# Kernel optimization log

Measured on AMD Instinct MI355X. Metric: run time of the kernel, lower is better.

The kernel has to match this reference:

```python
import jax, jax.numpy as jnp
import numpy as np

N, E, G = 10000, 80000, 32
Z, C, B, H = 10, 128, 8, 64
R_MAX = 5.0
AVG_NEIGH = 16.0
L_OFF = [0, 1, 4, 9, 16]  # slice offsets for l = 0..3 blocks of the SH vector


def real_sh(u):
    # Real spherical harmonics up to l=3, 'component' normalization (sum_m Y_lm^2 = 2l+1)
    x, y, z = u[:, 0], u[:, 1], u[:, 2]
    s3, s5, s15 = 3.0 ** 0.5, 5.0 ** 0.5, 15.0 ** 0.5
    cols = [
        jnp.ones_like(x),
        s3 * x, s3 * y, s3 * z,
        s15 * x * y, s15 * y * z, (s5 / 2) * (3 * z ** 2 - 1),
        s15 * x * z, (s15 / 2) * (x ** 2 - y ** 2),
        (70.0 ** 0.5 / 4) * (3 * x ** 2 * y - y ** 3),
        105.0 ** 0.5 * x * y * z,
        (42.0 ** 0.5 / 4) * y * (5 * z ** 2 - 1),
        (7.0 ** 0.5 / 2) * (5 * z ** 3 - 3 * z),
        (42.0 ** 0.5 / 4) * x * (5 * z ** 2 - 1),
        (105.0 ** 0.5 / 2) * z * (x ** 2 - y ** 2),
        (70.0 ** 0.5 / 4) * (x ** 3 - 3 * x * y ** 2),
    ]
    return jnp.stack(cols, axis=-1)  # [E, 16]


def poly_cutoff(x, p=5):
    f = (1.0 - (p + 1) * (p + 2) / 2 * x ** p
         + p * (p + 2) * x ** (p + 1)
         - p * (p + 1) / 2 * x ** (p + 2))
    return f * (x < 1.0).astype(f.dtype)


def setup_inputs() -> dict:
    key = jax.random.key(0)
    ks = jax.random.split(key, 20)
    vectors = jax.random.normal(ks[0], (E, 3), dtype=jnp.float32) * 1.5
    elem = jax.random.randint(ks[1], (N,), 0, Z)
    node_attrs = jax.nn.one_hot(elem, Z, dtype=jnp.float32)
    edge_index = jax.random.randint(ks[2], (2, E), 0, N).astype(jnp.int64)
    batch = jnp.sort(jax.random.randint(ks[3], (N,), 0, G)).astype(jnp.int64)

    def init(k, shape, fan_in):
        return jax.random.normal(k, shape, dtype=jnp.float32) / np.sqrt(fan_in)

    return {
        "vectors": vectors,
        "node_attrs": node_attrs,
        "W_embed": init(ks[4], (Z, C), Z),
        "atomic_energies": -jnp.arange(1, Z + 1, dtype=jnp.float32),
        "rw1": init(ks[5], (2, B, H), B),
        "rw2": init(ks[6], (2, H, H), H),
        "rw3": init(ks[7], (2, H, H), H),
        "rw4": init(ks[8], (2, H, 4 * C), H),
        "Wmix": init(ks[9], (2, 4, C, C), C),
        "U": init(ks[10], (2, Z, 4), Z),
        "Wprod": init(ks[11], (2, C, C), C),
        "Wsc": init(ks[12], (2, C, C), C),
        "Wro0": init(ks[13], (C, 1), C),
        "Wro1a": init(ks[14], (C, 16), C),
        "Wro1b": init(ks[15], (16, 1), 16),
        "scale": jnp.array([1.0], dtype=jnp.float32),
        "shift": jnp.array([0.0], dtype=jnp.float32),
        "edge_index": edge_index,
        "batch": batch,
    }


def reference(vectors, node_attrs, W_embed, atomic_energies, rw1, rw2, rw3, rw4,
              Wmix, U, Wprod, Wsc, Wro0, Wro1a, Wro1b, scale, shift,
              edge_index, batch):
    sender, receiver = edge_index[0], edge_index[1]
    r = jnp.linalg.norm(vectors, axis=-1)                     # [E]
    u = vectors / r[:, None]
    Y = real_sh(u)                                            # [E, 16]
    n = jnp.arange(1, B + 1, dtype=vectors.dtype)
    bessel = jnp.sqrt(2.0 / R_MAX) * jnp.sin(n[None] * jnp.pi * r[:, None] / R_MAX) / r[:, None]
    edge_feats = bessel * poly_cutoff(r / R_MAX)[:, None]     # [E, B]

    h = node_attrs @ W_embed                                  # [N, C] node embedding
    node_e0 = node_attrs @ atomic_energies                    # [N] atomic reference energies
    e0 = jax.ops.segment_sum(node_e0, batch, num_segments=G)  # [G]

    node_inter = jnp.zeros((node_attrs.shape[0],), dtype=vectors.dtype)
    for i in range(2):  # interaction layers (fixed small count)
        f = jax.nn.silu(edge_feats @ rw1[i])
        f = jax.nn.silu(f @ rw2[i])
        f = jax.nn.silu(f @ rw3[i])
        R_w = (f @ rw4[i]).reshape(-1, 4, C)                  # [E, 4, C] radial weights per l-path
        hs = h[sender]                                        # [E, C] edge gather
        A_parts = []
        for l in range(4):
            # channelwise tensor product (uvu): scalar node feats x Y_l -> l
            m = (R_w[:, l, :] * hs)[:, :, None] * Y[:, None, L_OFF[l]:L_OFF[l + 1]]  # [E, C, 2l+1]
            agg = jax.ops.segment_sum(m, receiver, num_segments=node_attrs.shape[0]) / AVG_NEIGH
            A_parts.append(jnp.einsum('ncm,cd->ndm', agg, Wmix[i, l]))
        # product basis: rotation-invariant powers per l, element-dependent contraction
        inv = jnp.stack([(p ** 2).sum(-1) for p in A_parts], axis=-1)  # [N, C, 4]
        w = node_attrs @ U[i]                                          # [N, 4]
        h = jnp.einsum('ncl,nl->nc', inv, w) @ Wprod[i] + h @ Wsc[i]   # product + residual sc
        if i == 0:
            node_inter = node_inter + (h @ Wro0)[:, 0]                 # linear readout
        else:
            node_inter = node_inter + (jax.nn.silu(h @ Wro1a) @ Wro1b)[:, 0]  # nonlinear readout
    node_inter = scale[0] * node_inter + shift[0]                       # scale-shift
    total = e0 + jax.ops.segment_sum(node_inter, batch, num_segments=G)
    return total  # [G] per-graph energies
```

## Files before the change

### kernel.cpp

```cpp
#include <hip/hip_runtime.h>

#define NN 10000
#define NE 80000
#define NG 32
#define NZ 10
#define NC 128
#define RMAXF 5.0f

typedef _Float16 f16;
typedef _Float16 half8 __attribute__((ext_vector_type(8)));
typedef float f32x4 __attribute__((ext_vector_type(4)));

__device__ __forceinline__ float silu_f(float x) {
    return x / (1.0f + __expf(-x));
}

__device__ __forceinline__ int clampi(int v, int lo, int hi) {
    return v < lo ? lo : (v > hi ? hi : v);
}

__device__ __forceinline__ uint4 pack8f(float4 a, float4 b) {
    union { f16 h[8]; uint4 u; } P;
    P.h[0] = (f16)a.x; P.h[1] = (f16)a.y; P.h[2] = (f16)a.z; P.h[3] = (f16)a.w;
    P.h[4] = (f16)b.x; P.h[5] = (f16)b.y; P.h[6] = (f16)b.z; P.h[7] = (f16)b.w;
    return P.u;
}

__global__ void zero_stuff(int* counts, int* cursor, float* out) {
    int i = blockIdx.x * blockDim.x + threadIdx.x;
    if (i < NN) { counts[i] = 0; cursor[i] = 0; }
    if (i < NG) out[i] = 0.0f;
}

__global__ void prep_weights(const float* __restrict__ Wmix, const float* __restrict__ Wprod,
                             const float* __restrict__ Wsc,
                             const float* __restrict__ rw2, const float* __restrict__ rw3,
                             const float* __restrict__ rw4,
                             f16* __restrict__ WmixT, f16* __restrict__ WprodT, f16* __restrict__ WscT,
                             f16* __restrict__ w2T, f16* __restrict__ w3T, f16* __restrict__ w4T) {
    int i = blockIdx.x * blockDim.x + threadIdx.x;
    if (i < 2 * 4 * 128 * 128) {
        int cc = i & 127, d = (i >> 7) & 127, g = i >> 14;
        WmixT[i] = (f16)Wmix[((size_t)g * 128 + cc) * 128 + d];
    }
    if (i < 2 * 128 * 128) {
        int cc = i & 127, d = (i >> 7) & 127, g = i >> 14;
        WprodT[i] = (f16)Wprod[((size_t)g * 128 + cc) * 128 + d];
        WscT[i]   = (f16)Wsc[((size_t)g * 128 + cc) * 128 + d];
    }
    if (i < 2 * 512 * 64) {
        int k = i & 63, j = (i >> 6) & 511, ly = i >> 15;
        w4T[i] = (f16)rw4[((size_t)ly * 64 + k) * 512 + j];
    }
    if (i < 2 * 64 * 64) {
        int k = i & 63, j = (i >> 6) & 63, ly = i >> 12;
        w2T[i] = (f16)rw2[((size_t)ly * 64 + k) * 64 + j];
        w3T[i] = (f16)rw3[((size_t)ly * 64 + k) * 64 + j];
    }
}

__global__ void node_init(const float* __restrict__ attrs, const float* __restrict__ W_embed,
                          const float* __restrict__ ae, const float* __restrict__ U,
                          float* __restrict__ h, float* __restrict__ node_e0, float* __restrict__ wU) {
    int gid = blockIdx.x * blockDim.x + threadIdx.x;
    if (gid >= NN * NC) return;
    int n = gid >> 7, c = gid & 127;
    float a[NZ];
#pragma unroll
    for (int z = 0; z < NZ; z++) a[z] = attrs[n * NZ + z];
    float acc = 0.f;
#pragma unroll
    for (int z = 0; z < NZ; z++) acc += a[z] * W_embed[z * NC + c];
    h[(size_t)n * NC + c] = acc;
    if (c == 0) {
        float e = 0.f;
#pragma unroll
        for (int z = 0; z < NZ; z++) e += a[z] * ae[z];
        node_e0[n] = e;
    }
    if (c < 8) {
        int i = c >> 2, l = c & 3;
        float s = 0.f;
#pragma unroll
        for (int z = 0; z < NZ; z++) s += a[z] * U[i * NZ * 4 + z * 4 + l];
        wU[(size_t)i * NN * 4 + n * 4 + l] = s;
    }
}

__global__ void edge_geom(const float* __restrict__ vec, float* __restrict__ Y, float* __restrict__ ef) {
    int e = blockIdx.x * blockDim.x + threadIdx.x;
    if (e >= NE) return;
    float vx = vec[e * 3 + 0], vy = vec[e * 3 + 1], vz = vec[e * 3 + 2];
    float r = sqrtf(vx * vx + vy * vy + vz * vz);
    float inv = 1.0f / r;
    float x = vx * inv, y = vy * inv, z = vz * inv;
    const float s3 = 1.7320508075688772f;
    const float s5 = 2.23606797749979f;
    const float s15 = 3.872983346207417f;
    const float c9 = 2.091650066335189f;
    const float c10 = 10.246950765959598f;
    const float c11 = 1.6201851746019651f;
    const float c12 = 1.3228756555322954f;
    const float c14 = 5.123475382979799f;
    float o[16];
    o[0] = 1.0f;
    o[1] = s3 * x; o[2] = s3 * y; o[3] = s3 * z;
    o[4] = s15 * x * y; o[5] = s15 * y * z; o[6] = 0.5f * s5 * (3.f * z * z - 1.f);
    o[7] = s15 * x * z; o[8] = 0.5f * s15 * (x * x - y * y);
    o[9] = c9 * (3.f * x * x * y - y * y * y);
    o[10] = c10 * x * y * z;
    o[11] = c11 * y * (5.f * z * z - 1.f);
    o[12] = c12 * (5.f * z * z * z - 3.f * z);
    o[13] = c11 * x * (5.f * z * z - 1.f);
    o[14] = c14 * z * (x * x - y * y);
    o[15] = c9 * (x * x * x - 3.f * x * y * y);
#pragma unroll
    for (int m = 0; m < 16; m++) Y[(size_t)e * 16 + m] = o[m];
    float xc = r / RMAXF;
    float cut = 0.0f;
    if (xc < 1.0f) {
        float x5 = xc * xc * xc * xc * xc;
        cut = 1.0f - 21.0f * x5 + 35.0f * x5 * xc - 15.0f * x5 * xc * xc;
    }
    float pref = sqrtf(2.0f / RMAXF) * inv * cut;
#pragma unroll
    for (int b = 0; b < 8; b++) {
        float arg = (float)(b + 1) * 3.14159265358979323846f * r / RMAXF;
        ef[(size_t)e * 8 + b] = pref * sinf(arg);
    }
}

__global__ void hist_recv(const int* __restrict__ recv, int* __restrict__ counts) {
    int e = blockIdx.x * blockDim.x + threadIdx.x;
    if (e < NE) atomicAdd(&counts[clampi(recv[e], 0, NN - 1)], 1);
}

__global__ void scan_counts(const int* __restrict__ counts, int* __restrict__ rowstart) {
    __shared__ int part[1024];
    int t = threadIdx.x;
    const int CH = 10;
    int base = t * CH;
    int loc[CH];
    int s = 0;
#pragma unroll
    for (int j = 0; j < CH; j++) {
        int v = (base + j < NN) ? counts[base + j] : 0;
        loc[j] = s; s += v;
    }
    part[t] = s;
    __syncthreads();
    for (int off = 1; off < 1024; off <<= 1) {
        int v = (t >= off) ? part[t - off] : 0;
        __syncthreads();
        part[t] += v;
        __syncthreads();
    }
    int chunk = (t > 0) ? part[t - 1] : 0;
#pragma unroll
    for (int j = 0; j < CH; j++)
        if (base + j < NN) rowstart[base + j] = chunk + loc[j];
    if (t == 0) rowstart[NN] = part[1023];
}

__global__ void scatter_edges(const int* __restrict__ recv, const int* __restrict__ rowstart,
                              int* __restrict__ cursor, int* __restrict__ elist) {
    int e = blockIdx.x * blockDim.x + threadIdx.x;
    if (e < NE) {
        int r = clampi(recv[e], 0, NN - 1);
        int p = atomicAdd(&cursor[r], 1);
        int slot = clampi(rowstart[r] + p, 0, NE - 1);
        elist[slot] = e;
    }
}

__global__ __launch_bounds__(256) void edge_mlp(const float* __restrict__ ef,
                                                const float* __restrict__ w1,
                                                const f16* __restrict__ w2T, const f16* __restrict__ w3T,
                                                const f16* __restrict__ w4T,
                                                f16* __restrict__ Rw) {
    __shared__ __align__(16) char L[8192 * 2 + 16384];
    char* X1 = L;
    char* X2 = L + 8192;
    char* X4 = L + 16384;

    int tid = threadIdx.x;
    int lane = tid & 63;
    int w = tid >> 6;
    int ln = lane & 15, kq = lane >> 4;
    int eb = blockIdx.x * 64;

    {
        int jb = w * 16;
        const float4* efv = (const float4*)(ef + (size_t)(eb + lane) * 8);
        float4 ea = efv[0], eb4 = efv[1];
        float in8[8] = {ea.x, ea.y, ea.z, ea.w, eb4.x, eb4.y, eb4.z, eb4.w};
        f16 pk[16];
#pragma unroll
        for (int j = 0; j < 16; j++) {
            float a = 0.f;
#pragma unroll
            for (int b = 0; b < 8; b++) a += in8[b] * w1[b * 64 + jb + j];
            pk[j] = (f16)silu_f(a);
        }
        int base = lane * 128 + jb * 2;
#pragma unroll
        for (int t = 0; t < 2; t++) {
            int byte = (base + t * 16) ^ ((lane & 7) << 4);
            *(uint4*)(X1 + byte) = ((uint4*)pk)[t];
        }
    }
    __syncthreads();

    {
        half8 a[2];
#pragma unroll
        for (int kc = 0; kc < 2; kc++) {
            int byte = ((w * 16 + ln) * 128 + kc * 64 + kq * 16) ^ ((ln & 7) << 4);
            a[kc] = *(const half8*)(X1 + byte);
        }
#pragma unroll
        for (int nt = 0; nt < 4; nt++) {
            f32x4 acc = {0.f, 0.f, 0.f, 0.f};
#pragma unroll
            for (int kc = 0; kc < 2; kc++) {
                half8 b = *(const half8*)(w2T + (nt * 16 + ln) * 64 + kc * 32 + kq * 8);
                acc = __builtin_amdgcn_mfma_f32_16x16x32_f16(a[kc], b, acc, 0, 0, 0);
            }
#pragma unroll
            for (int r = 0; r < 4; r++) {
                int row = w * 16 + kq * 4 + r;
                int byte = (row * 128 + (nt * 16 + ln) * 2) ^ ((row & 7) << 4);
                *(f16*)(X2 + byte) = (f16)silu_f(acc[r]);
            }
        }
    }
    __syncthreads();

    {
        half8 a[2];
#pragma unroll
        for (int kc = 0; kc < 2; kc++) {
            int byte = ((w * 16 + ln) * 128 + kc * 64 + kq * 16) ^ ((ln & 7) << 4);
            a[kc] = *(const half8*)(X2 + byte);
        }
#pragma unroll
        for (int nt = 0; nt < 4; nt++) {
            f32x4 acc = {0.f, 0.f, 0.f, 0.f};
#pragma unroll
            for (int kc = 0; kc < 2; kc++) {
                half8 b = *(const half8*)(w3T + (nt * 16 + ln) * 64 + kc * 32 + kq * 8);
                acc = __builtin_amdgcn_mfma_f32_16x16x32_f16(a[kc], b, acc, 0, 0, 0);
            }
#pragma unroll
            for (int r = 0; r < 4; r++) {
                int row = w * 16 + kq * 4 + r;
                int byte = (row * 128 + (nt * 16 + ln) * 2) ^ ((row & 7) << 4);
                *(f16*)(X1 + byte) = (f16)silu_f(acc[r]);
            }
        }
    }
    __syncthreads();

    half8 a3[2];
#pragma unroll
    for (int kc = 0; kc < 2; kc++) {
        int byte = ((w * 16 + ln) * 128 + kc * 64 + kq * 16) ^ ((ln & 7) << 4);
        a3[kc] = *(const half8*)(X1 + byte);
    }
    for (int q = 0; q < 4; q++) {
#pragma unroll
        for (int nt = 0; nt < 8; nt++) {
            f32x4 acc = {0.f, 0.f, 0.f, 0.f};
#pragma unroll
            for (int kc = 0; kc < 2; kc++) {
                half8 b = *(const half8*)(w4T + ((q * 8 + nt) * 16 + ln) * 64 + kc * 32 + kq * 8);
                acc = __builtin_amdgcn_mfma_f32_16x16x32_f16(a3[kc], b, acc, 0, 0, 0);
            }
#pragma unroll
            for (int r = 0; r < 4; r++) {
                int row = w * 16 + kq * 4 + r;
                int byte = (row * 256 + (nt * 16 + ln) * 2) ^ ((row & 15) << 4);
                *(f16*)(X4 + byte) = (f16)acc[r];
            }
        }
#pragma unroll
        for (int it = 0; it < 4; it++) {
            int i = it * 64 + lane;
            int row = w * 16 + (i >> 4);
            int chunk = i & 15;
            int byte = (row * 256 + chunk * 16) ^ ((row & 15) << 4);
            uint4 v = *(const uint4*)(X4 + byte);
            *(uint4*)(Rw + (size_t)(eb + row) * 512 + q * 128 + chunk * 8) = v;
        }
    }
}

__global__ __launch_bounds__(256) void agg_only(const int* __restrict__ rowstart, const int* __restrict__ elist,
                                                const int* __restrict__ send, const float* __restrict__ h_in,
                                                const f16* __restrict__ Rw, const float* __restrict__ Y,
                                                f16* __restrict__ aggH) {
    __shared__ int eL[64], sL[64];
    int n = blockIdx.x, tid = threadIdx.x;
    int c = tid & 127, mh = tid >> 7;
    float acc[8];
#pragma unroll
    for (int q = 0; q < 8; q++) acc[q] = 0.f;
    int beg = rowstart[n], end = rowstart[n + 1];
    for (int base = beg; base < end; base += 64) {
        int cnt = min(64, end - base);
        __syncthreads();
        if (tid < cnt) {
            int e = clampi(elist[base + tid], 0, NE - 1);
            eL[tid] = e;
            sL[tid] = clampi(send[e], 0, NN - 1);
        }
        __syncthreads();
        for (int idx = 0; idx < cnt; idx++) {
            int e = eL[idx];
            int s = sL[idx];
            float hs = h_in[(size_t)s * NC + c];
            const f16* rwp = Rw + (size_t)e * 512;
            float y[8];
#pragma unroll
            for (int q = 0; q < 8; q++) y[q] = Y[(size_t)e * 16 + mh * 8 + q];
            if (mh == 0) {
                float p0 = (float)rwp[c] * hs;
                float p1 = (float)rwp[128 + c] * hs;
                float p2 = (float)rwp[256 + c] * hs;
                acc[0] += p0 * y[0];
                acc[1] += p1 * y[1]; acc[2] += p1 * y[2]; acc[3] += p1 * y[3];
                acc[4] += p2 * y[4]; acc[5] += p2 * y[5]; acc[6] += p2 * y[6]; acc[7] += p2 * y[7];
            } else {
                float p2 = (float)rwp[256 + c] * hs;
                float p3 = (float)rwp[384 + c] * hs;
                acc[0] += p2 * y[0];
#pragma unroll
                for (int q = 1; q < 8; q++) acc[q] += p3 * y[q];
            }
        }
    }
    const float inv16 = 1.0f / 16.0f;
#pragma unroll
    for (int q = 0; q < 8; q++)
        aggH[(size_t)n * 2048 + (size_t)(mh * 8 + q) * NC + c] = (f16)(acc[q] * inv16);
}

__global__ __launch_bounds__(256) void mix_mfma(
    const f16* __restrict__ aggH, const f16* __restrict__ WmixT,
    const float* __restrict__ wU, const float* __restrict__ h_in,
    const f16* __restrict__ WprodT, const f16* __restrict__ WscT,
    const float* __restrict__ Wro0, const float* __restrict__ Wro1a, const float* __restrict__ Wro1b,
    float* __restrict__ h_out, float* __restrict__ ni, int layer)
{
    __shared__ __align__(16) char Lb[65536 + 8192 + 256 + 1024];
    float* invwL = (float*)(Lb + 65536);
    float* wUL   = (float*)(Lb + 65536 + 8192);
    float* p16L  = (float*)(Lb + 65536 + 8192 + 256);
    f16* houtH   = (f16*)(Lb + 65536);

    int tid = threadIdx.x;
    int nb = blockIdx.x * 16;
    int lane = tid & 63;
    int w = tid >> 6;
    int ln = lane & 15, kq = lane >> 4;

    {
        const uint4* src = (const uint4*)(aggH + (size_t)nb * 2048);
        for (int i = tid; i < 4096; i += 256) {
            int byte = i * 16;
            int node = byte >> 12;
            int sw = byte ^ ((node & 7) << 4);
            *(uint4*)(Lb + sw) = src[i];
        }
    }
    if (tid < 64) wUL[tid] = wU[(size_t)nb * 4 + tid];
    for (int i = tid; i < 2048; i += 256) invwL[i] = 0.f;
    __syncthreads();

    float invwacc[32];
#pragma unroll
    for (int i = 0; i < 32; i++) invwacc[i] = 0.f;
#pragma unroll
    for (int i = 0; i < 4; i++) {
        int m = w * 4 + i;
        int l = (m == 0) ? 0 : (m < 4) ? 1 : (m < 9) ? 2 : 3;
        half8 a[4];
#pragma unroll
        for (int k = 0; k < 4; k++) {
            int byte = (ln * 16 + m) * 256 + (k * 32 + kq * 8) * 2;
            byte ^= (ln & 7) << 4;
            a[k] = *(const half8*)(Lb + byte);
        }
        const f16* Bt = WmixT + ((size_t)(layer * 4 + l) << 14);
#pragma unroll
        for (int nt = 0; nt < 8; nt++) {
            f32x4 acc = {0.f, 0.f, 0.f, 0.f};
#pragma unroll
            for (int k = 0; k < 4; k++) {
                half8 b = *(const half8*)(Bt + (nt * 16 + ln) * 128 + k * 32 + kq * 8);
                acc = __builtin_amdgcn_mfma_f32_16x16x32_f16(a[k], b, acc, 0, 0, 0);
            }
#pragma unroll
            for (int r = 0; r < 4; r++) {
                int nd = kq * 4 + r;
                float v = acc[r];
                invwacc[nt * 4 + r] += v * v * wUL[nd * 4 + l];
            }
        }
    }
#pragma unroll
    for (int nt = 0; nt < 8; nt++)
#pragma unroll
        for (int r = 0; r < 4; r++)
            atomicAdd(&invwL[(kq * 4 + r) * 128 + nt * 16 + ln], invwacc[nt * 4 + r]);
    __syncthreads();

    {
        int node = tid >> 4, ch = tid & 15;
        int byte = (node * 256 + ch * 16) ^ ((node & 7) << 4);
        float4 v0 = *(float4*)&invwL[node * 128 + ch * 8];
        float4 v1 = *(float4*)&invwL[node * 128 + ch * 8 + 4];
        *(uint4*)(Lb + byte) = pack8f(v0, v1);
        const float4* hp = (const float4*)(h_in + (size_t)(nb + node) * 128 + ch * 8);
        float4 g0 = hp[0], g1 = hp[1];
        *(uint4*)(Lb + 4096 + byte) = pack8f(g0, g1);
    }
    __syncthreads();

    {
        half8 ai[4], ah[4];
#pragma unroll
        for (int k = 0; k < 4; k++) {
            int byte = (ln * 256 + (k * 32 + kq * 8) * 2) ^ ((ln & 7) << 4);
            ai[k] = *(const half8*)(Lb + byte);
            ah[k] = *(const half8*)(Lb + 4096 + byte);
        }
        const f16* Bp = WprodT + ((size_t)layer << 14);
        const f16* Bs = WscT + ((size_t)layer << 14);
#pragma unroll
        for (int j = 0; j < 2; j++) {
            int nt = w * 2 + j;
            f32x4 acc = {0.f, 0.f, 0.f, 0.f};
#pragma unroll
            for (int k = 0; k < 4; k++) {
                half8 b = *(const half8*)(Bp + (nt * 16 + ln) * 128 + k * 32 + kq * 8);
                acc = __builtin_amdgcn_mfma_f32_16x16x32_f16(ai[k], b, acc, 0, 0, 0);
            }
#pragma unroll
            for (int k = 0; k < 4; k++) {
                half8 b = *(const half8*)(Bs + (nt * 16 + ln) * 128 + k * 32 + kq * 8);
                acc = __builtin_amdgcn_mfma_f32_16x16x32_f16(ah[k], b, acc, 0, 0, 0);
            }
#pragma unroll
            for (int r = 0; r < 4; r++) {
                int node = kq * 4 + r;
                int d = nt * 16 + ln;
                h_out[(size_t)(nb + node) * 128 + d] = acc[r];
                houtH[node * 128 + d] = (f16)acc[r];
            }
        }
    }
    __syncthreads();

    int rn = tid >> 4, rj = tid & 15;
    if (layer == 0) {
        float s = 0.f;
        for (int cc = rj; cc < 128; cc += 16) s += (float)houtH[rn * 128 + cc] * Wro0[cc];
        p16L[tid] = s;
    } else {
        float s = 0.f;
        for (int cc = 0; cc < 128; cc++) s += (float)houtH[rn * 128 + cc] * Wro1a[cc * 16 + rj];
        s = silu_f(s);
        p16L[tid] = s * Wro1b[rj];
    }
    __syncthreads();
    if (tid < 16) {
        float t = 0.f;
#pragma unroll
        for (int j = 0; j < 16; j++) t += p16L[tid * 16 + j];
        ni[nb + tid] = (layer == 0) ? t : (ni[nb + tid] + t);
    }
}

__global__ void finalize(const float* __restrict__ node_e0, const float* __restrict__ ni,
                         const int* __restrict__ batch, const float* __restrict__ scale,
                         const float* __restrict__ shift, float* __restrict__ out) {
    __shared__ float bins[NG];
    int tid = threadIdx.x;
    if (tid < NG) bins[tid] = 0.f;
    __syncthreads();
    int n = blockIdx.x * blockDim.x + tid;
    if (n < NN) {
        float v = node_e0[n] + scale[0] * ni[n] + shift[0];
        atomicAdd(&bins[clampi(batch[n], 0, NG - 1)], v);
    }
    __syncthreads();
    if (tid < NG) atomicAdd(&out[tid], bins[tid]);
}

extern "C" void kernel_launch(void* const* d_in, const int* in_sizes, int n_in,
                              void* d_out, int out_size, void* d_ws, size_t ws_size,
                              hipStream_t stream) {
    (void)in_sizes; (void)n_in; (void)out_size; (void)ws_size;
    const float* vectors = (const float*)d_in[0];
    const float* attrs   = (const float*)d_in[1];
    const float* W_embed = (const float*)d_in[2];
    const float* ae      = (const float*)d_in[3];
    const float* rw1     = (const float*)d_in[4];
    const float* rw2     = (const float*)d_in[5];
    const float* rw3     = (const float*)d_in[6];
    const float* rw4     = (const float*)d_in[7];
    const float* Wmix    = (const float*)d_in[8];
    const float* U       = (const float*)d_in[9];
    const float* Wprod   = (const float*)d_in[10];
    const float* Wsc     = (const float*)d_in[11];
    const float* Wro0    = (const float*)d_in[12];
    const float* Wro1a   = (const float*)d_in[13];
    const float* Wro1b   = (const float*)d_in[14];
    const float* scale   = (const float*)d_in[15];
    const float* shift   = (const float*)d_in[16];
    const int* eidx      = (const int*)d_in[17];
    const int* batch     = (const int*)d_in[18];
    float* out = (float*)d_out;

    char* w = (char*)d_ws;
    size_t off = 0;
    auto alloc = [&](size_t bytes) -> void* {
        void* p = (void*)(w + off);
        off += (bytes + 255) & ~(size_t)255;
        return p;
    };
    float* Y       = (float*)alloc((size_t)NE * 16 * 4);
    float* ef      = (float*)alloc((size_t)NE * 8 * 4);
    f16*   Rw      = (f16*)  alloc((size_t)NE * 512 * 2);
    f16*   aggH    = (f16*)  alloc((size_t)NN * 2048 * 2);
    float* hA      = (float*)alloc((size_t)NN * NC * 4);
    float* hB      = (float*)alloc((size_t)NN * NC * 4);
    float* wU      = (float*)alloc((size_t)2 * NN * 4 * 4);
    float* node_e0 = (float*)alloc((size_t)NN * 4);
    float* ni      = (float*)alloc((size_t)NN * 4);
    f16*   WmixT   = (f16*)  alloc((size_t)2 * 4 * 128 * 128 * 2);
    f16*   WprodT  = (f16*)  alloc((size_t)2 * 128 * 128 * 2);
    f16*   WscT    = (f16*)  alloc((size_t)2 * 128 * 128 * 2);
    f16*   w2T     = (f16*)  alloc((size_t)2 * 64 * 64 * 2);
    f16*   w3T     = (f16*)  alloc((size_t)2 * 64 * 64 * 2);
    f16*   w4T     = (f16*)  alloc((size_t)2 * 512 * 64 * 2);
    int* counts    = (int*)alloc((size_t)NN * 4);
    int* rowstart  = (int*)alloc((size_t)(NN + 1) * 4);
    int* cursor    = (int*)alloc((size_t)NN * 4);
    int* elist     = (int*)alloc((size_t)NE * 4);

    const int* send = eidx;
    const int* recv = eidx + NE;
    zero_stuff<<<(NN + 255) / 256, 256, 0, stream>>>(counts, cursor, out);
    prep_weights<<<512, 256, 0, stream>>>(Wmix, Wprod, Wsc, rw2, rw3, rw4,
                                          WmixT, WprodT, WscT, w2T, w3T, w4T);
    node_init<<<(NN * NC + 255) / 256, 256, 0, stream>>>(attrs, W_embed, ae, U, hA, node_e0, wU);
    edge_geom<<<(NE + 255) / 256, 256, 0, stream>>>(vectors, Y, ef);
    hist_recv<<<(NE + 255) / 256, 256, 0, stream>>>(recv, counts);
    scan_counts<<<1, 1024, 0, stream>>>(counts, rowstart);
    scatter_edges<<<(NE + 255) / 256, 256, 0, stream>>>(recv, rowstart, cursor, elist);

    float* hcur = hA;
    float* hnext = hB;
    for (int layer = 0; layer < 2; layer++) {
        edge_mlp<<<NE / 64, 256, 0, stream>>>(
            ef, rw1 + layer * 8 * 64,
            w2T + (size_t)layer * 64 * 64, w3T + (size_t)layer * 64 * 64,
            w4T + (size_t)layer * 512 * 64, Rw);
        agg_only<<<NN, 256, 0, stream>>>(rowstart, elist, send, hcur, Rw, Y, aggH);
        mix_mfma<<<NN / 16, 256, 0, stream>>>(
            aggH, WmixT, wU + (size_t)layer * NN * 4, hcur,
            WprodT, WscT, Wro0, Wro1a, Wro1b, hnext, ni, layer);
        float* t = hcur; hcur = hnext; hnext = t;
    }
    finalize<<<(NN + 255) / 256, 256, 0, stream>>>(node_e0, ni, batch, scale, shift, out);
}
```

Baseline: 413.3 us.

## Load aggregated features directly into registers and double mix_mfma block width

mix_mfma now runs with 512 threads (8 waves), each wave handling two m components instead of four, and loads its A fragments directly from global memory rather than staging the 64KB aggH tile through LDS. Shared memory per block drops from about 74KB to about 21KB, which allows more blocks per CU and removes one staging pass and barrier. The Wprod/Wsc stage now gives one output tile to each of the 8 waves. The risk is that direct global A loads are less coalesced, and the extra waves add some idle threads in the final readout stages.

```diff
diff --git a/kernel.cpp b/kernel.cpp
--- a/kernel.cpp
+++ b/kernel.cpp
@@ -345,18 +345,20 @@
         aggH[(size_t)n * 2048 + (size_t)(mh * 8 + q) * NC + c] = (f16)(acc[q] * inv16);
 }
 
-__global__ __launch_bounds__(256) void mix_mfma(
+__global__ __launch_bounds__(512) void mix_mfma(
     const f16* __restrict__ aggH, const f16* __restrict__ WmixT,
     const float* __restrict__ wU, const float* __restrict__ h_in,
     const f16* __restrict__ WprodT, const f16* __restrict__ WscT,
     const float* __restrict__ Wro0, const float* __restrict__ Wro1a, const float* __restrict__ Wro1b,
     float* __restrict__ h_out, float* __restrict__ ni, int layer)
 {
-    __shared__ __align__(16) char Lb[65536 + 8192 + 256 + 1024];
-    float* invwL = (float*)(Lb + 65536);
-    float* wUL   = (float*)(Lb + 65536 + 8192);
-    float* p16L  = (float*)(Lb + 65536 + 8192 + 256);
-    f16* houtH   = (f16*)(Lb + 65536);
+    __shared__ __align__(16) char Lb[21760];
+    f16*   invwH = (f16*)(Lb);
+    f16*   hH    = (f16*)(Lb + 4096);
+    float* invwL = (float*)(Lb + 8192);
+    float* wUL   = (float*)(Lb + 16384);
+    float* p16L  = (float*)(Lb + 16640);
+    f16*   houtH = (f16*)(Lb + 17664);
 
     int tid = threadIdx.x;
     int nb = blockIdx.x * 16;
@@ -364,48 +366,43 @@
     int w = tid >> 6;
     int ln = lane & 15, kq = lane >> 4;
 
+    for (int i = tid; i < 2048; i += 512) invwL[i] = 0.f;
+    if (tid < 64) wUL[tid] = wU[(size_t)nb * 4 + tid];
+    __syncthreads();
+
+    int m0 = 2 * w, m1 = 2 * w + 1;
+    int l0 = (m0 == 0) ? 0 : (m0 < 4) ? 1 : (m0 < 9) ? 2 : 3;
+    int l1 = (m1 < 4) ? 1 : (m1 < 9) ? 2 : 3;
+    half8 a0[4], a1[4];
     {
-        const uint4* src = (const uint4*)(aggH + (size_t)nb * 2048);
-        for (int i = tid; i < 4096; i += 256) {
-            int byte = i * 16;
-            int node = byte >> 12;
-            int sw = byte ^ ((node & 7) << 4);
-            *(uint4*)(Lb + sw) = src[i];
-        }
-    }
-    if (tid < 64) wUL[tid] = wU[(size_t)nb * 4 + tid];
-    for (int i = tid; i < 2048; i += 256) invwL[i] = 0.f;
-    __syncthreads();
-
+        const f16* arow = aggH + (size_t)(nb + ln) * 2048 + kq * 8;
+#pragma unroll
+        for (int k = 0; k < 4; k++) {
+            a0[k] = *(const half8*)(arow + m0 * 128 + k * 32);
+            a1[k] = *(const half8*)(arow + m1 * 128 + k * 32);
+        }
+    }
+    const f16* Bt0 = WmixT + ((size_t)(layer * 4 + l0) << 14);
+    const f16* Bt1 = WmixT + ((size_t)(layer * 4 + l1) << 14);
     float invwacc[32];
 #pragma unroll
     for (int i = 0; i < 32; i++) invwacc[i] = 0.f;
 #pragma unroll
-    for (int i = 0; i < 4; i++) {
-        int m = w * 4 + i;
-        int l = (m == 0) ? 0 : (m < 4) ? 1 : (m < 9) ? 2 : 3;
-        half8 a[4];
+    for (int nt = 0; nt < 8; nt++) {
+        f32x4 acc0 = {0.f, 0.f, 0.f, 0.f}, acc1 = {0.f, 0.f, 0.f, 0.f};
 #pragma unroll
         for (int k = 0; k < 4; k++) {
-            int byte = (ln * 16 + m) * 256 + (k * 32 + kq * 8) * 2;
-            byte ^= (ln & 7) << 4;
-            a[k] = *(const half8*)(Lb + byte);
-        }
-        const f16* Bt = WmixT + ((size_t)(layer * 4 + l) << 14);
-#pragma unroll
-        for (int nt = 0; nt < 8; nt++) {
-            f32x4 acc = {0.f, 0.f, 0.f, 0.f};
-#pragma unroll
-            for (int k = 0; k < 4; k++) {
-                half8 b = *(const half8*)(Bt + (nt * 16 + ln) * 128 + k * 32 + kq * 8);
-                acc = __builtin_amdgcn_mfma_f32_16x16x32_f16(a[k], b, acc, 0, 0, 0);
-            }
-#pragma unroll
-            for (int r = 0; r < 4; r++) {
-                int nd = kq * 4 + r;
-                float v = acc[r];
-                invwacc[nt * 4 + r] += v * v * wUL[nd * 4 + l];
-            }
+            int bo = (nt * 16 + ln) * 128 + k * 32 + kq * 8;
+            half8 b0 = *(const half8*)(Bt0 + bo);
+            half8 b1 = *(const half8*)(Bt1 + bo);
+            acc0 = __builtin_amdgcn_mfma_f32_16x16x32_f16(a0[k], b0, acc0, 0, 0, 0);
+            acc1 = __builtin_amdgcn_mfma_f32_16x16x32_f16(a1[k], b1, acc1, 0, 0, 0);
+        }
+#pragma unroll
+        for (int r = 0; r < 4; r++) {
+            int nd = kq * 4 + r;
+            invwacc[nt * 4 + r] += acc0[r] * acc0[r] * wUL[nd * 4 + l0]
+                                 + acc1[r] * acc1[r] * wUL[nd * 4 + l1];
         }
     }
 #pragma unroll
@@ -415,15 +412,15 @@
             atomicAdd(&invwL[(kq * 4 + r) * 128 + nt * 16 + ln], invwacc[nt * 4 + r]);
     __syncthreads();
 
-    {
+    if (tid < 256) {
         int node = tid >> 4, ch = tid & 15;
         int byte = (node * 256 + ch * 16) ^ ((node & 7) << 4);
         float4 v0 = *(float4*)&invwL[node * 128 + ch * 8];
         float4 v1 = *(float4*)&invwL[node * 128 + ch * 8 + 4];
-        *(uint4*)(Lb + byte) = pack8f(v0, v1);
+        *(uint4*)((char*)invwH + byte) = pack8f(v0, v1);
         const float4* hp = (const float4*)(h_in + (size_t)(nb + node) * 128 + ch * 8);
         float4 g0 = hp[0], g1 = hp[1];
-        *(uint4*)(Lb + 4096 + byte) = pack8f(g0, g1);
+        *(uint4*)((char*)hH + byte) = pack8f(g0, g1);
     }
     __syncthreads();
 
@@ -432,46 +429,44 @@
 #pragma unroll
         for (int k = 0; k < 4; k++) {
             int byte = (ln * 256 + (k * 32 + kq * 8) * 2) ^ ((ln & 7) << 4);
-            ai[k] = *(const half8*)(Lb + byte);
-            ah[k] = *(const half8*)(Lb + 4096 + byte);
+            ai[k] = *(const half8*)((char*)invwH + byte);
+            ah[k] = *(const half8*)((char*)hH + byte);
         }
         const f16* Bp = WprodT + ((size_t)layer << 14);
         const f16* Bs = WscT + ((size_t)layer << 14);
-#pragma unroll
-        for (int j = 0; j < 2; j++) {
-            int nt = w * 2 + j;
-            f32x4 acc = {0.f, 0.f, 0.f, 0.f};
-#pragma unroll
-            for (int k = 0; k < 4; k++) {
-                half8 b = *(const half8*)(Bp + (nt * 16 + ln) * 128 + k * 32 + kq * 8);
-                acc = __builtin_amdgcn_mfma_f32_16x16x32_f16(ai[k], b, acc, 0, 0, 0);
-            }
-#pragma unroll
-            for (int k = 0; k < 4; k++) {
-                half8 b = *(const half8*)(Bs + (nt * 16 + ln) * 128 + k * 32 + kq * 8);
-                acc = __builtin_amdgcn_mfma_f32_16x16x32_f16(ah[k], b, acc, 0, 0, 0);
-            }
-#pragma unroll
-            for (int r = 0; r < 4; r++) {
-                int node = kq * 4 + r;
-                int d = nt * 16 + ln;
-                h_out[(size_t)(nb + node) * 128 + d] = acc[r];
-                houtH[node * 128 + d] = (f16)acc[r];
-            }
-        }
-    }
-    __syncthreads();
-
-    int rn = tid >> 4, rj = tid & 15;
-    if (layer == 0) {
-        float s = 0.f;
-        for (int cc = rj; cc < 128; cc += 16) s += (float)houtH[rn * 128 + cc] * Wro0[cc];
-        p16L[tid] = s;
-    } else {
-        float s = 0.f;
-        for (int cc = 0; cc < 128; cc++) s += (float)houtH[rn * 128 + cc] * Wro1a[cc * 16 + rj];
-        s = silu_f(s);
-        p16L[tid] = s * Wro1b[rj];
+        f32x4 acc = {0.f, 0.f, 0.f, 0.f};
+#pragma unroll
+        for (int k = 0; k < 4; k++) {
+            half8 b = *(const half8*)(Bp + (w * 16 + ln) * 128 + k * 32 + kq * 8);
+            acc = __builtin_amdgcn_mfma_f32_16x16x32_f16(ai[k], b, acc, 0, 0, 0);
+        }
+#pragma unroll
+        for (int k = 0; k < 4; k++) {
+            half8 b = *(const half8*)(Bs + (w * 16 + ln) * 128 + k * 32 + kq * 8);
+            acc = __builtin_amdgcn_mfma_f32_16x16x32_f16(ah[k], b, acc, 0, 0, 0);
+        }
+#pragma unroll
+        for (int r = 0; r < 4; r++) {
+            int node = kq * 4 + r;
+            int d = w * 16 + ln;
+            h_out[(size_t)(nb + node) * 128 + d] = acc[r];
+            houtH[node * 128 + d] = (f16)acc[r];
+        }
+    }
+    __syncthreads();
+
+    if (tid < 256) {
+        int rn = tid >> 4, rj = tid & 15;
+        if (layer == 0) {
+            float s = 0.f;
+            for (int cc = rj; cc < 128; cc += 16) s += (float)houtH[rn * 128 + cc] * Wro0[cc];
+            p16L[tid] = s;
+        } else {
+            float s = 0.f;
+            for (int cc = 0; cc < 128; cc++) s += (float)houtH[rn * 128 + cc] * Wro1a[cc * 16 + rj];
+            s = silu_f(s);
+            p16L[tid] = s * Wro1b[rj];
+        }
     }
     __syncthreads();
     if (tid < 16) {
@@ -569,7 +564,7 @@
             w2T + (size_t)layer * 64 * 64, w3T + (size_t)layer * 64 * 64,
             w4T + (size_t)layer * 512 * 64, Rw);
         agg_only<<<NN, 256, 0, stream>>>(rowstart, elist, send, hcur, Rw, Y, aggH);
-        mix_mfma<<<NN / 16, 256, 0, stream>>>(
+        mix_mfma<<<NN / 16, 512, 0, stream>>>(
             aggH, WmixT, wU + (size_t)layer * NN * 4, hcur,
             WprodT, WscT, Wro0, Wro1a, Wro1b, hnext, ni, layer);
         float* t = hcur; hcur = hnext; hnext = t;
```

After: 473.8 us. +14.6%, slower.
